# Kernel optimization log

Measured on AMD Instinct MI355X. Metric: run time of the kernel, lower is better.

## Reference

```python
import jax, jax.numpy as jnp
import numpy as np

B, T, D = 4096, 200, 64
H = 32  # hidden units of score MLP
NEG_INF = jnp.float32(-2**32 + 1)


def setup_inputs() -> dict:
    key = jax.random.key(0)
    k1, k2, k3, k4, k5 = jax.random.split(key, 5)
    query = jax.random.normal(k1, (B, 1, D), dtype=jnp.float32)
    keys = jax.random.normal(k2, (B, T, D), dtype=jnp.float32)
    mask = jax.random.randint(k3, (B, T), 0, 2) > 0
    mask = mask.at[:, 0].set(True)  # ensure at least one valid key per row
    # Glorot-normal-ish init for the tiny score MLP
    W1 = jax.random.normal(k4, (3 * D, H), dtype=jnp.float32) * jnp.sqrt(2.0 / (3 * D + H))
    b1 = jnp.zeros((H,), dtype=jnp.float32)
    W2 = jax.random.normal(k5, (H, 1), dtype=jnp.float32) * jnp.sqrt(2.0 / (H + 1))
    b2 = jnp.zeros((1,), dtype=jnp.float32)
    return {"query": query, "keys": keys, "mask": mask,
            "W1": W1, "b1": b1, "W2": W2, "b2": b2}


def reference(query, keys, mask, W1, b1, W2, b2):
    b, t, d = keys.shape
    q = jnp.broadcast_to(query, (b, t, d))            # tile query over seq
    att_in = jnp.concatenate([q, keys, q - keys], axis=-1)   # [B,T,3D]
    h = jax.nn.sigmoid(att_in @ W1 + b1)              # [B,T,H]
    score = (h @ W2 + b2)[..., 0]                     # [B,T]
    score = jnp.where(mask, score, NEG_INF)
    w = jax.nn.softmax(score, axis=-1)                # [B,T]
    out = jnp.einsum('bt,btd->bd', w, keys)           # weighted key sum
    return out[:, None, :]                            # [B,1,D]
```

## Files before the change

kernel.cpp:

```cpp
#include <hip/hip_runtime.h>
#include <hip/hip_bf16.h>


#define B 4096
#define T 200
#define D 64
#define H 32


__global__ __launch_bounds__(256) void prep_kernel(
        const float* __restrict__ W1,
        const float* __restrict__ b1,
        const float* __restrict__ query,
        float*       __restrict__ ws)
{
    int n = blockIdx.x * 256 + threadIdx.x;
    if (blockIdx.x < 8) {
        int j = n >> 6;
        int i = n & 63;
        ws[n] = W1[(64 + i) * H + j] - W1[(128 + i) * H + j];
    } else {
        int m = n - 2048;
        int b = m >> 5;
        int j = m & 31;
        const float* qb = query + (size_t)b * D;
        float acc = b1[j];
        #pragma unroll 8
        for (int i = 0; i < D; ++i)
            acc = fmaf(qb[i], W1[i * H + j] + W1[(128 + i) * H + j], acc);
        ws[2048 + m] = acc;
    }
}

__global__ __launch_bounds__(256, 5) void attn_pool_kernel(
        const float* __restrict__ keys,
        const int*   __restrict__ mask,
        const float* __restrict__ wkT,
        const float* __restrict__ qa_all,
        const float* __restrict__ W2,
        float*       __restrict__ out)
{
    __shared__ float wts[T];
    __shared__ float redmax[4];
    __shared__ float redsum[4];
    __shared__ float part[256];

    const int tid  = threadIdx.x;
    const int b    = blockIdx.x;
    const int t    = tid;
    const int wv   = tid >> 6;
    const int lane = tid & 63;

    const float* qa = qa_all + (size_t)b * H;

    float s = -INFINITY;
    if (t < T) {
        float4 kreg[16];
        const float4* kp = reinterpret_cast<const float4*>(keys + (size_t)b * (T * D) + t * D);
        #pragma unroll
        for (int i4 = 0; i4 < 16; ++i4)
            kreg[i4] = kp[i4];

        float sc = 0.0f;
        #pragma unroll 2
        for (int j = 0; j < H; ++j) {
            const float* wrow = &wkT[j * D];
            float a0 = 0.f, a1 = 0.f, a2 = 0.f, a3 = 0.f;
            #pragma unroll
            for (int i4 = 0; i4 < 16; i4 += 4) {
                float4 k0 = kreg[i4 + 0];
                a0 = fmaf(k0.x, wrow[(i4+0)*4+0], a0);
                a0 = fmaf(k0.y, wrow[(i4+0)*4+1], a0);
                a0 = fmaf(k0.z, wrow[(i4+0)*4+2], a0);
                a0 = fmaf(k0.w, wrow[(i4+0)*4+3], a0);
                float4 k1 = kreg[i4 + 1];
                a1 = fmaf(k1.x, wrow[(i4+1)*4+0], a1);
                a1 = fmaf(k1.y, wrow[(i4+1)*4+1], a1);
                a1 = fmaf(k1.z, wrow[(i4+1)*4+2], a1);
                a1 = fmaf(k1.w, wrow[(i4+1)*4+3], a1);
                float4 k2 = kreg[i4 + 2];
                a2 = fmaf(k2.x, wrow[(i4+2)*4+0], a2);
                a2 = fmaf(k2.y, wrow[(i4+2)*4+1], a2);
                a2 = fmaf(k2.z, wrow[(i4+2)*4+2], a2);
                a2 = fmaf(k2.w, wrow[(i4+2)*4+3], a2);
                float4 k3 = kreg[i4 + 3];
                a3 = fmaf(k3.x, wrow[(i4+3)*4+0], a3);
                a3 = fmaf(k3.y, wrow[(i4+3)*4+1], a3);
                a3 = fmaf(k3.z, wrow[(i4+3)*4+2], a3);
                a3 = fmaf(k3.w, wrow[(i4+3)*4+3], a3);
            }
            float x = qa[j] + ((a0 + a1) + (a2 + a3));
            float e = exp2f(-x * 1.44269504088896340736f);
            float hval = __builtin_amdgcn_rcpf(1.0f + e);
            sc = fmaf(hval, W2[j], sc);
        }
        s = (mask[(size_t)b * T + t] != 0) ? sc : -4294967295.0f;
    }

    float m = s;
    #pragma unroll
    for (int off = 32; off >= 1; off >>= 1)
        m = fmaxf(m, __shfl_xor(m, off, 64));
    if (lane == 0) redmax[wv] = m;
    __syncthreads();
    m = fmaxf(fmaxf(redmax[0], redmax[1]), fmaxf(redmax[2], redmax[3]));

    float e = (t < T) ? exp2f((s - m) * 1.44269504088896340736f) : 0.0f;
    float tot = e;
    #pragma unroll
    for (int off = 32; off >= 1; off >>= 1)
        tot += __shfl_xor(tot, off, 64);
    if (lane == 0) redsum[wv] = tot;
    __syncthreads();
    tot = (redsum[0] + redsum[1]) + (redsum[2] + redsum[3]);

    if (t < T) wts[t] = e * __builtin_amdgcn_rcpf(tot);
    __syncthreads();

    {
        const float* krow = keys + (size_t)b * (T * D);
        float acc = 0.0f;
        const int t0 = wv * 50;
        #pragma unroll 5
        for (int tt = t0; tt < t0 + 50; ++tt)
            acc = fmaf(wts[tt], krow[tt * D + lane], acc);
        part[wv * 64 + lane] = acc;
    }
    __syncthreads();
    if (tid < 64) {
        out[(size_t)b * D + tid] =
            ((part[tid] + part[64 + tid]) + (part[128 + tid] + part[192 + tid]));
    }
}

extern "C" void kernel_launch(void* const* d_in, const int* in_sizes, int n_in,
                              void* d_out, int out_size, void* d_ws, size_t ws_size,
                              hipStream_t stream) {
    const float* query = (const float*)d_in[0];
    const float* keys  = (const float*)d_in[1];
    const int*   mask  = (const int*)d_in[2];
    const float* W1    = (const float*)d_in[3];
    const float* b1    = (const float*)d_in[4];
    const float* W2    = (const float*)d_in[5];

    float* ws  = (float*)d_ws;
    float* wkT = ws;
    float* qa  = ws + 2048;

    prep_kernel<<<8 + (B * H) / 256, 256, 0, stream>>>(W1, b1, query, ws);
    attn_pool_kernel<<<B, 256, 0, stream>>>(keys, mask, wkT, qa, W2, (float*)d_out);
}
```

Measured before the change: 334.0 us.

## Compute score MLP with bf16 MFMA from LDS-staged keys

Replaces the per-thread fp32 FMA loop for the keys·W1 projection with bf16 MFMA 16x16x32 instructions. Keys are converted to bf16 and staged in padded LDS, and the prep kernel pre-swizzles the weight difference into MFMA B-fragment layout. The aim is to cut the ALU-bound score computation, at the cost of bf16 rounding in the scores and an extra LDS staging pass with one more barrier. The weighted sum still rereads keys from global memory.

```diff
diff --git a/kernel.cpp b/kernel.cpp
--- a/kernel.cpp
+++ b/kernel.cpp
@@ -6,124 +6,159 @@
 #define T 200
 #define D 64
 #define H 32
+#define TP 208
+#define KP 72
+
+typedef __attribute__((ext_vector_type(8))) short short8;
+typedef __attribute__((ext_vector_type(4))) float f32x4;
 
 
 __global__ __launch_bounds__(256) void prep_kernel(
         const float* __restrict__ W1,
         const float* __restrict__ b1,
         const float* __restrict__ query,
-        float*       __restrict__ ws)
+        float*       __restrict__ qa_ws,
+        unsigned short* __restrict__ wkf)
 {
-    int n = blockIdx.x * 256 + threadIdx.x;
-    if (blockIdx.x < 8) {
-        int j = n >> 6;
-        int i = n & 63;
-        ws[n] = W1[(64 + i) * H + j] - W1[(128 + i) * H + j];
-    } else {
-        int m = n - 2048;
-        int b = m >> 5;
-        int j = m & 31;
+    int blk = blockIdx.x;
+    int n = blk * 256 + threadIdx.x;
+    if (blk < (B * H) / 256) {
+        int b = n >> 5;
+        int j = n & 31;
         const float* qb = query + (size_t)b * D;
         float acc = b1[j];
         #pragma unroll 8
         for (int i = 0; i < D; ++i)
             acc = fmaf(qb[i], W1[i * H + j] + W1[(128 + i) * H + j], acc);
-        ws[2048 + m] = acc;
+        qa_ws[n] = acc;
+    } else {
+        int m = n - (B * H);
+        int e  = m & 7;
+        int l  = (m >> 3) & 63;
+        int fs = m >> 9;
+        int ntile = fs >> 1, kstep = fs & 1;
+        int k = kstep * 32 + (l >> 4) * 8 + e;
+        int j = ntile * 16 + (l & 15);
+        float v = W1[(64 + k) * H + j] - W1[(128 + k) * H + j];
+        __hip_bfloat16 hv = __float2bfloat16(v);
+        wkf[m] = __builtin_bit_cast(unsigned short, hv);
     }
 }
 
 __global__ __launch_bounds__(256, 5) void attn_pool_kernel(
         const float* __restrict__ keys,
         const int*   __restrict__ mask,
-        const float* __restrict__ wkT,
+        const unsigned short* __restrict__ wkf,
         const float* __restrict__ qa_all,
         const float* __restrict__ W2,
         float*       __restrict__ out)
 {
-    __shared__ float wts[T];
-    __shared__ float redmax[4];
-    __shared__ float redsum[4];
-    __shared__ float part[256];
+    __shared__ unsigned short kt[TP * KP];
+    __shared__ float sc_lds[TP];
+    __shared__ float red[8];
 
     const int tid  = threadIdx.x;
     const int b    = blockIdx.x;
-    const int t    = tid;
     const int wv   = tid >> 6;
     const int lane = tid & 63;
+    const int quad = lane >> 4;
+    const int l15  = lane & 15;
+
+    const float4* kp = reinterpret_cast<const float4*>(keys + (size_t)b * (T * D));
+    for (int idx = tid; idx < (T * D) / 4; idx += 256) {
+        float4 v = kp[idx];
+        int t  = idx >> 4;
+        int i4 = idx & 15;
+        __hip_bfloat16 h0 = __float2bfloat16(v.x);
+        __hip_bfloat16 h1 = __float2bfloat16(v.y);
+        __hip_bfloat16 h2 = __float2bfloat16(v.z);
+        __hip_bfloat16 h3 = __float2bfloat16(v.w);
+        ushort4 u;
+        u.x = __builtin_bit_cast(unsigned short, h0);
+        u.y = __builtin_bit_cast(unsigned short, h1);
+        u.z = __builtin_bit_cast(unsigned short, h2);
+        u.w = __builtin_bit_cast(unsigned short, h3);
+        *reinterpret_cast<ushort4*>(&kt[t * KP + i4 * 4]) = u;
+    }
+    if (tid < 144) {
+        ushort4 z; z.x = z.y = z.z = z.w = 0;
+        *reinterpret_cast<ushort4*>(&kt[T * KP + tid * 4]) = z;
+    }
+
+    const short8* wf = reinterpret_cast<const short8*>(wkf);
+    short8 bfrag[4];
+    #pragma unroll
+    for (int fs = 0; fs < 4; ++fs)
+        bfrag[fs] = wf[fs * 64 + lane];
 
     const float* qa = qa_all + (size_t)b * H;
+    float qa0 = qa[l15];
+    float qa1 = qa[16 + l15];
+    float w20 = W2[l15];
+    float w21 = W2[16 + l15];
 
-    float s = -INFINITY;
-    if (t < T) {
-        float4 kreg[16];
-        const float4* kp = reinterpret_cast<const float4*>(keys + (size_t)b * (T * D) + t * D);
+    __syncthreads();
+
+    for (int m0 = wv; m0 < TP / 16; m0 += 4) {
+        const int trow = m0 * 16 + l15;
+        short8 a0 = *reinterpret_cast<const short8*>(&kt[trow * KP + quad * 8]);
+        short8 a1 = *reinterpret_cast<const short8*>(&kt[trow * KP + 32 + quad * 8]);
+
+        f32x4 acc0 = {0.f, 0.f, 0.f, 0.f};
+        f32x4 acc1 = {0.f, 0.f, 0.f, 0.f};
+        acc0 = __builtin_amdgcn_mfma_f32_16x16x32_bf16(a0, bfrag[0], acc0, 0, 0, 0);
+        acc0 = __builtin_amdgcn_mfma_f32_16x16x32_bf16(a1, bfrag[1], acc0, 0, 0, 0);
+        acc1 = __builtin_amdgcn_mfma_f32_16x16x32_bf16(a0, bfrag[2], acc1, 0, 0, 0);
+        acc1 = __builtin_amdgcn_mfma_f32_16x16x32_bf16(a1, bfrag[3], acc1, 0, 0, 0);
+
         #pragma unroll
-        for (int i4 = 0; i4 < 16; ++i4)
-            kreg[i4] = kp[i4];
+        for (int r = 0; r < 4; ++r) {
+            float x0 = acc0[r] + qa0;
+            float x1 = acc1[r] + qa1;
+            float s0 = __builtin_amdgcn_rcpf(1.0f + exp2f(-x0 * 1.44269504088896340736f));
+            float s1 = __builtin_amdgcn_rcpf(1.0f + exp2f(-x1 * 1.44269504088896340736f));
+            float p = fmaf(s0, w20, s1 * w21);
+            #pragma unroll
+            for (int off = 1; off <= 8; off <<= 1)
+                p += __shfl_xor(p, off, 64);
+            if (l15 == 0)
+                sc_lds[m0 * 16 + quad * 4 + r] = p;
+        }
+    }
+    __syncthreads();
 
-        float sc = 0.0f;
-        #pragma unroll 2
-        for (int j = 0; j < H; ++j) {
-            const float* wrow = &wkT[j * D];
-            float a0 = 0.f, a1 = 0.f, a2 = 0.f, a3 = 0.f;
-            #pragma unroll
-            for (int i4 = 0; i4 < 16; i4 += 4) {
-                float4 k0 = kreg[i4 + 0];
-                a0 = fmaf(k0.x, wrow[(i4+0)*4+0], a0);
-                a0 = fmaf(k0.y, wrow[(i4+0)*4+1], a0);
-                a0 = fmaf(k0.z, wrow[(i4+0)*4+2], a0);
-                a0 = fmaf(k0.w, wrow[(i4+0)*4+3], a0);
-                float4 k1 = kreg[i4 + 1];
-                a1 = fmaf(k1.x, wrow[(i4+1)*4+0], a1);
-                a1 = fmaf(k1.y, wrow[(i4+1)*4+1], a1);
-                a1 = fmaf(k1.z, wrow[(i4+1)*4+2], a1);
-                a1 = fmaf(k1.w, wrow[(i4+1)*4+3], a1);
-                float4 k2 = kreg[i4 + 2];
-                a2 = fmaf(k2.x, wrow[(i4+2)*4+0], a2);
-                a2 = fmaf(k2.y, wrow[(i4+2)*4+1], a2);
-                a2 = fmaf(k2.z, wrow[(i4+2)*4+2], a2);
-                a2 = fmaf(k2.w, wrow[(i4+2)*4+3], a2);
-                float4 k3 = kreg[i4 + 3];
-                a3 = fmaf(k3.x, wrow[(i4+3)*4+0], a3);
-                a3 = fmaf(k3.y, wrow[(i4+3)*4+1], a3);
-                a3 = fmaf(k3.z, wrow[(i4+3)*4+2], a3);
-                a3 = fmaf(k3.w, wrow[(i4+3)*4+3], a3);
-            }
-            float x = qa[j] + ((a0 + a1) + (a2 + a3));
-            float e = exp2f(-x * 1.44269504088896340736f);
-            float hval = __builtin_amdgcn_rcpf(1.0f + e);
-            sc = fmaf(hval, W2[j], sc);
-        }
-        s = (mask[(size_t)b * T + t] != 0) ? sc : -4294967295.0f;
-    }
+    const int t = tid;
+    float s = (t < T) ? ((mask[(size_t)b * T + t] != 0) ? sc_lds[t] : -4294967295.0f)
+                      : -INFINITY;
 
     float m = s;
     #pragma unroll
     for (int off = 32; off >= 1; off >>= 1)
         m = fmaxf(m, __shfl_xor(m, off, 64));
-    if (lane == 0) redmax[wv] = m;
+    if (lane == 0) red[wv] = m;
     __syncthreads();
-    m = fmaxf(fmaxf(redmax[0], redmax[1]), fmaxf(redmax[2], redmax[3]));
+    m = fmaxf(fmaxf(red[0], red[1]), fmaxf(red[2], red[3]));
 
     float e = (t < T) ? exp2f((s - m) * 1.44269504088896340736f) : 0.0f;
     float tot = e;
     #pragma unroll
     for (int off = 32; off >= 1; off >>= 1)
         tot += __shfl_xor(tot, off, 64);
-    if (lane == 0) redsum[wv] = tot;
+    if (lane == 0) red[4 + wv] = tot;
     __syncthreads();
-    tot = (redsum[0] + redsum[1]) + (redsum[2] + redsum[3]);
+    tot = (red[4] + red[5]) + (red[6] + red[7]);
 
-    if (t < T) wts[t] = e * __builtin_amdgcn_rcpf(tot);
+    if (t < T) sc_lds[t] = e * __builtin_amdgcn_rcpf(tot);
     __syncthreads();
 
+    float* part = reinterpret_cast<float*>(kt);
     {
         const float* krow = keys + (size_t)b * (T * D);
         float acc = 0.0f;
         const int t0 = wv * 50;
         #pragma unroll 5
         for (int tt = t0; tt < t0 + 50; ++tt)
-            acc = fmaf(wts[tt], krow[tt * D + lane], acc);
+            acc = fmaf(sc_lds[tt], krow[tt * D + lane], acc);
         part[wv * 64 + lane] = acc;
     }
     __syncthreads();
@@ -143,10 +178,9 @@
     const float* b1    = (const float*)d_in[4];
     const float* W2    = (const float*)d_in[5];
 
-    float* ws  = (float*)d_ws;
-    float* wkT = ws;
-    float* qa  = ws + 2048;
+    float* qa = (float*)d_ws;
+    unsigned short* wkf = (unsigned short*)(qa + B * H);
 
-    prep_kernel<<<8 + (B * H) / 256, 256, 0, stream>>>(W1, b1, query, ws);
-    attn_pool_kernel<<<B, 256, 0, stream>>>(keys, mask, wkT, qa, W2, (float*)d_out);
+    prep_kernel<<<(B * H) / 256 + 8, 256, 0, stream>>>(W1, b1, query, qa, wkf);
+    attn_pool_kernel<<<B, 256, 0, stream>>>(keys, mask, wkf, qa, W2, (float*)d_out);
 }
```

Result: no change. 335.9 us (+0.6%).
